# Kernel tuning notes

Measured on AMD Instinct MI355X. Metric: run time of the kernel, lower is better.

The kernel has to match this reference:

```python
import jax, jax.numpy as jnp
import numpy as np

H, C, DK = 4, 63, 64   # n_head, context_size, d_k
NF = H * DK            # n_feat = 256


def setup_inputs() -> dict:
    key = jax.random.key(0)
    ks = jax.random.split(key, 7)
    B, T = 2, 4096
    query = jax.random.normal(ks[0], (B, T, NF), jnp.float32)
    key_t = jax.random.normal(ks[1], (B, T, NF), jnp.float32)   # dummy, unused
    value = jax.random.normal(ks[2], (B, T, NF), jnp.float32)
    mask = jnp.ones((B, 1, T), jnp.bool_)                       # dummy, unused
    s = 1.0 / np.sqrt(NF).astype(np.float32)
    w1 = jax.random.normal(ks[3], (NF, NF), jnp.float32) * s
    w2 = jax.random.normal(ks[4], (H * C, NF), jnp.float32) * s
    w3 = jax.random.normal(ks[5], (NF, NF), jnp.float32) * s
    w_out = jax.random.normal(ks[6], (NF, NF), jnp.float32) * s
    return {"query": query, "key": key_t, "value": value, "mask": mask,
            "w1": w1, "w2": w2, "w3": w3, "w_out": w_out}


def reference(query, key, value, mask, w1, w2, w3, w_out):
    # key and mask are dummies (unused), matching the original module.
    B, T, _ = query.shape
    half = (C - 1) // 2

    q = query @ w1.T                                            # (B,T,NF)
    # synthesized band scores: (B,H,T,C)
    weight = (jax.nn.relu(q) @ w2.T).reshape(B, T, H, C).transpose(0, 2, 1, 3)

    # band geometry: score(i, j) lives at offset k = j - i + half, |j-i| <= half
    j_idx = jnp.arange(T)[:, None] + jnp.arange(C)[None, :] - half   # (T,C)
    valid = (j_idx >= 0) & (j_idx < T)                               # (T,C)
    scores = jnp.where(valid[None, None], weight, -jnp.inf)
    p_attn = jax.nn.softmax(scores, axis=-1)                         # (B,H,T,C)

    v = (value @ w3.T).reshape(B, T, H, DK).transpose(0, 2, 1, 3)    # (B,H,T,DK)
    jc = jnp.clip(j_idx, 0, T - 1)                                   # safe gather idx
    windows = v[:, :, jc, :]                                         # (B,H,T,C,DK)
    x = jnp.einsum('bhtc,bhtcd->bhtd', p_attn, windows)              # (B,H,T,DK)

    x = x.transpose(0, 2, 1, 3).reshape(B, T, NF)
    return x @ w_out.T
```

## Files before the change

kernel.cpp:

```cpp
#include <hip/hip_runtime.h>
#include <hip/hip_bf16.h>
#include <math.h>

typedef _Float16 f16x8 __attribute__((ext_vector_type(8)));
typedef _Float16 f16x4 __attribute__((ext_vector_type(4)));
typedef float    f32x4 __attribute__((ext_vector_type(4)));

__device__ __host__ __forceinline__ int swz(int ch, int row) {
    return (ch & 24) | ((ch & 7) ^ (row & 7));
}
__device__ __forceinline__ f32x4 mfma16(f16x8 a, f16x8 b, f32x4 c) {
    return __builtin_amdgcn_mfma_f32_16x16x32_f16(a, b, c, 0, 0, 0);
}
__device__ __forceinline__ f16x8 cvt8(float4 lo, float4 hi) {
    f16x8 r = { (_Float16)lo.x, (_Float16)lo.y, (_Float16)lo.z, (_Float16)lo.w,
                (_Float16)hi.x, (_Float16)hi.y, (_Float16)hi.z, (_Float16)hi.w };
    return r;
}

__global__ __launch_bounds__(256) void convw(const float* __restrict__ w1,
                                             const float* __restrict__ w2,
                                             const float* __restrict__ w3,
                                             const float* __restrict__ wo,
                                             _Float16* __restrict__ p1,
                                             _Float16* __restrict__ p2,
                                             _Float16* __restrict__ p3,
                                             _Float16* __restrict__ po) {
    int gid = blockIdx.x * 256 + threadIdx.x;
    int widx = gid >> 13;
    int r    = gid & 8191;
    int lane = r & 63;
    int ks   = (r >> 6) & 7;
    int nblk = r >> 9;
    int n  = nblk * 16 + (lane & 15);
    int kc = (ks * 4 + (lane >> 4)) * 8;
    const float* src = widx == 0 ? w1 : widx == 1 ? w2 : widx == 2 ? w3 : wo;
    _Float16*    dst = widx == 0 ? p1 : widx == 1 ? p2 : widx == 2 ? p3 : po;
    f16x8 h = {};
    if (!(widx == 1 && n >= 252)) {
        float4 lo = *(const float4*)&src[n * 256 + kc];
        float4 hi = *(const float4*)&src[n * 256 + kc + 4];
        h = cvt8(lo, hi);
    }
    *(f16x8*)&dst[r * 8] = h;
}

__global__ __launch_bounds__(1024, 4) void mono(const float* __restrict__ query,
                                                const float* __restrict__ value,
                                                const _Float16* __restrict__ w1p,
                                                const _Float16* __restrict__ w2p,
                                                const _Float16* __restrict__ w3p,
                                                const _Float16* __restrict__ wop,
                                                float* __restrict__ outp) {
    __shared__ __align__(16) _Float16 RA[16384];
    __shared__ __align__(16) _Float16 RB[8192];
    __shared__ __align__(16) _Float16 Vs[24576];
    __shared__ __align__(16) _Float16 vwT[26624];

    const int tid = threadIdx.x, lane = tid & 63, wid = tid >> 6;
    const int bidr = blockIdx.x;
    const int work = (bidr & 7) * 32 + (bidr >> 3);
    const int b   = work >> 7;
    const int t0  = (work & 127) * 32;
    const size_t rowb = (size_t)b * 4096;

    _Float16* Aq = RA;
    _Float16* Qr = RA + 8192;
    _Float16* Pl = RA;
    _Float16* sc = RB;
    _Float16* xb = RB;

    {
        int row = tid >> 5, ch = tid & 31;
        const float* qp = &query[(rowb + t0 + row) * 256 + ch * 8];
        float4 qlo = *(const float4*)qp, qhi = *(const float4*)(qp + 4);
        float4 vlo[3], vhi[3];
        #pragma unroll
        for (int it = 0; it < 3; ++it) {
            int slot = it * 1024 + tid;
            int vrow = slot >> 5, vch = slot & 31;
            int jl = t0 - 32 + vrow;
            jl = jl < 0 ? 0 : (jl > 4095 ? 4095 : jl);
            const float* p = &value[(rowb + jl) * 256 + vch * 8];
            vlo[it] = *(const float4*)p;
            vhi[it] = *(const float4*)(p + 4);
        }
        *(f16x8*)&Aq[row * 256 + swz(ch, row) * 8] = cvt8(qlo, qhi);
        #pragma unroll
        for (int it = 0; it < 3; ++it) {
            int slot = it * 1024 + tid;
            int vrow = slot >> 5, vch = slot & 31;
            *(f16x8*)&Vs[vrow * 256 + swz(vch, vrow) * 8] = cvt8(vlo[it], vhi[it]);
        }
    }
    __syncthreads();

    {
        f16x8 bfa[8];
        #pragma unroll
        for (int ks = 0; ks < 8; ++ks)
            bfa[ks] = *(const f16x8*)&w1p[((wid * 8 + ks) * 64 + lane) * 8];
        f32x4 acc[2] = {};
        #pragma unroll
        for (int ks = 0; ks < 8; ++ks) {
            int chn = ks * 4 + (lane >> 4);
            #pragma unroll
            for (int i = 0; i < 2; ++i) {
                int row = i * 16 + (lane & 15);
                f16x8 af = *(const f16x8*)&Aq[row * 256 + swz(chn, row) * 8];
                acc[i] = mfma16(af, bfa[ks], acc[i]);
            }
        }
        const int n = wid * 16 + (lane & 15);
        #pragma unroll
        for (int i = 0; i < 2; ++i)
            #pragma unroll
            for (int r = 0; r < 4; ++r) {
                int row = i * 16 + ((lane >> 4) << 2) + r;
                float v = fmaxf(acc[i][r], 0.f);
                Qr[row * 256 + swz(n >> 3, row) * 8 + (n & 7)] = (_Float16)v;
            }
    }
    __syncthreads();

    {
        f16x8 bfa[8];
        #pragma unroll
        for (int ks = 0; ks < 8; ++ks)
            bfa[ks] = *(const f16x8*)&w2p[((wid * 8 + ks) * 64 + lane) * 8];
        f32x4 acc[2] = {};
        #pragma unroll
        for (int ks = 0; ks < 8; ++ks) {
            int chn = ks * 4 + (lane >> 4);
            #pragma unroll
            for (int i = 0; i < 2; ++i) {
                int row = i * 16 + (lane & 15);
                f16x8 af = *(const f16x8*)&Qr[row * 256 + swz(chn, row) * 8];
                acc[i] = mfma16(af, bfa[ks], acc[i]);
            }
        }
        const int n = wid * 16 + (lane & 15);
        #pragma unroll
        for (int i = 0; i < 2; ++i)
            #pragma unroll
            for (int r = 0; r < 4; ++r) {
                int row = i * 16 + ((lane >> 4) << 2) + r;
                sc[row * 256 + n] = (_Float16)acc[i][r];
            }
    }

    {
        f16x8 bfa[8];
        #pragma unroll
        for (int ks = 0; ks < 8; ++ks)
            bfa[ks] = *(const f16x8*)&w3p[((wid * 8 + ks) * 64 + lane) * 8];
        f32x4 a3[6] = {};
        #pragma unroll
        for (int ks = 0; ks < 8; ++ks) {
            int chn = ks * 4 + (lane >> 4);
            #pragma unroll
            for (int mi = 0; mi < 6; ++mi) {
                int row = mi * 16 + (lane & 15);
                f16x8 af = *(const f16x8*)&Vs[row * 256 + swz(chn, row) * 8];
                a3[mi] = mfma16(af, bfa[ks], a3[mi]);
            }
        }
        const int d = wid * 16 + (lane & 15);
        #pragma unroll
        for (int mi = 0; mi < 6; ++mi) {
            int jw = mi * 16 + ((lane >> 4) << 2);
            f16x4 h = { (_Float16)a3[mi][0], (_Float16)a3[mi][1],
                        (_Float16)a3[mi][2], (_Float16)a3[mi][3] };
            *(f16x4*)&vwT[d * 104 + jw] = h;
        }
    }
    __syncthreads();

    const int h = wid >> 2, q = wid & 3;
    #pragma unroll
    for (int it = 0; it < 2; ++it) {
        int s = it * 64 + lane;
        if (s < 104) {
            int rr = h * 32 + q * 8 + s / 13;
            int cc = s % 13;
            f16x8 z = {};
            *(f16x8*)&Pl[rr * 104 + cc * 8] = z;
        }
    }

    {
        const int hf = lane >> 5, c = lane & 31;
        #pragma unroll
        for (int i = 0; i < 4; ++i) {
            int tl = q * 8 + 2 * i + hf;
            int t  = t0 + tl;
            int c1 = c + 32;
            int j0 = t + c - 31, j1 = t + c1 - 31;
            bool ok0 = (j0 >= 0) && (j0 < 4096);
            bool ok1 = (c1 < 63) && (j1 >= 0) && (j1 < 4096);
            float s0 = ok0 ? (float)sc[tl * 256 + h * 63 + c]  : -INFINITY;
            float s1 = ok1 ? (float)sc[tl * 256 + h * 63 + c1] : -INFINITY;
            float mx = fmaxf(s0, s1);
            #pragma unroll
            for (int off = 16; off > 0; off >>= 1) mx = fmaxf(mx, __shfl_xor(mx, off));
            float e0 = ok0 ? __expf(s0 - mx) : 0.f;
            float e1 = ok1 ? __expf(s1 - mx) : 0.f;
            float sum = e0 + e1;
            #pragma unroll
            for (int off = 16; off > 0; off >>= 1) sum += __shfl_xor(sum, off);
            float inv = 1.0f / sum;
            Pl[(h * 32 + tl) * 104 + (tl + c + 1)] = (_Float16)(e0 * inv);
            if (c1 < 63) Pl[(h * 32 + tl) * 104 + (tl + c1 + 1)] = (_Float16)(e1 * inv);
        }
    }
    __syncthreads();

    {
        const int th = (wid >> 1) & 1, dh = wid & 1;
        f32x4 xa[2] = {};
        #pragma unroll
        for (int ks = 0; ks < 3; ++ks) {
            int chn = ks * 4 + (lane >> 4);
            f16x8 af = *(const f16x8*)&Pl[(h * 32 + th * 16 + (lane & 15)) * 104 + chn * 8];
            #pragma unroll
            for (int j = 0; j < 2; ++j) {
                f16x8 bf = *(const f16x8*)&vwT[(h * 64 + dh * 32 + j * 16 + (lane & 15)) * 104 + chn * 8];
                xa[j] = mfma16(af, bf, xa[j]);
            }
        }
        #pragma unroll
        for (int j = 0; j < 2; ++j)
            #pragma unroll
            for (int r = 0; r < 4; ++r) {
                int row = th * 16 + ((lane >> 4) << 2) + r;
                int n   = h * 64 + dh * 32 + j * 16 + (lane & 15);
                xb[row * 256 + swz(n >> 3, row) * 8 + (n & 7)] = (_Float16)xa[j][r];
            }
    }
    __syncthreads();

    {
        f16x8 bfa[8];
        #pragma unroll
        for (int ks = 0; ks < 8; ++ks)
            bfa[ks] = *(const f16x8*)&wop[((wid * 8 + ks) * 64 + lane) * 8];
        f32x4 oa[2] = {};
        #pragma unroll
        for (int ks = 0; ks < 8; ++ks) {
            int chn = ks * 4 + (lane >> 4);
            #pragma unroll
            for (int i = 0; i < 2; ++i) {
                int row = i * 16 + (lane & 15);
                f16x8 af = *(const f16x8*)&xb[row * 256 + swz(chn, row) * 8];
                oa[i] = mfma16(af, bfa[ks], oa[i]);
            }
        }
        const int n = wid * 16 + (lane & 15);
        #pragma unroll
        for (int i = 0; i < 2; ++i)
            #pragma unroll
            for (int r = 0; r < 4; ++r) {
                int m = t0 + i * 16 + ((lane >> 4) << 2) + r;
                outp[(rowb + m) * 256 + n] = oa[i][r];
            }
    }
}

extern "C" void kernel_launch(void* const* d_in, const int* in_sizes, int n_in,
                              void* d_out, int out_size, void* d_ws, size_t ws_size,
                              hipStream_t stream) {
    const float* query = (const float*)d_in[0];
    const float* value = (const float*)d_in[2];
    const float* w1    = (const float*)d_in[4];
    const float* w2    = (const float*)d_in[5];
    const float* w3    = (const float*)d_in[6];
    const float* w_out = (const float*)d_in[7];

    char* ws = (char*)d_ws;
    _Float16* w1p = (_Float16*)ws;
    _Float16* w2p = w1p + 65536;
    _Float16* w3p = w2p + 65536;
    _Float16* wop = w3p + 65536;

    convw<<<dim3(128), dim3(256), 0, stream>>>(w1, w2, w3, w_out, w1p, w2p, w3p, wop);
    mono<<<dim3(256), dim3(1024), 0, stream>>>(query, value, w1p, w2p, w3p, wop, (float*)d_out);
}
```

Baseline: 25.63 us.

## Fuse weight conversion into main kernel with atomic flag handoff

Removes the separate weight-conversion launch. The first 64 blocks of the main kernel now convert and pack the weights to fp16 and signal completion by incrementing a global atomic counter. Every block spins on that counter after staging its query and value tiles, which hides the conversion behind the input loads. The value projection is also re-tiled so each wave computes 3x2 MFMA tiles instead of 6x1, reusing A fragments across two B fragments. This relies on all producer blocks being co-resident, or the spin-wait can deadlock, and it adds a memset launch.

New measurement: 37.51 us. 1.46x slower.

```diff
diff --git a/kernel.cpp b/kernel.cpp
--- a/kernel.cpp
+++ b/kernel.cpp
@@ -5,6 +5,8 @@
 typedef _Float16 f16x8 __attribute__((ext_vector_type(8)));
 typedef _Float16 f16x4 __attribute__((ext_vector_type(4)));
 typedef float    f32x4 __attribute__((ext_vector_type(4)));
+
+#define NPROD 64
 
 __device__ __host__ __forceinline__ int swz(int ch, int row) {
     return (ch & 24) | ((ch & 7) ^ (row & 7));
@@ -18,39 +20,17 @@
     return r;
 }
 
-__global__ __launch_bounds__(256) void convw(const float* __restrict__ w1,
-                                             const float* __restrict__ w2,
-                                             const float* __restrict__ w3,
-                                             const float* __restrict__ wo,
-                                             _Float16* __restrict__ p1,
-                                             _Float16* __restrict__ p2,
-                                             _Float16* __restrict__ p3,
-                                             _Float16* __restrict__ po) {
-    int gid = blockIdx.x * 256 + threadIdx.x;
-    int widx = gid >> 13;
-    int r    = gid & 8191;
-    int lane = r & 63;
-    int ks   = (r >> 6) & 7;
-    int nblk = r >> 9;
-    int n  = nblk * 16 + (lane & 15);
-    int kc = (ks * 4 + (lane >> 4)) * 8;
-    const float* src = widx == 0 ? w1 : widx == 1 ? w2 : widx == 2 ? w3 : wo;
-    _Float16*    dst = widx == 0 ? p1 : widx == 1 ? p2 : widx == 2 ? p3 : po;
-    f16x8 h = {};
-    if (!(widx == 1 && n >= 252)) {
-        float4 lo = *(const float4*)&src[n * 256 + kc];
-        float4 hi = *(const float4*)&src[n * 256 + kc + 4];
-        h = cvt8(lo, hi);
-    }
-    *(f16x8*)&dst[r * 8] = h;
-}
-
 __global__ __launch_bounds__(1024, 4) void mono(const float* __restrict__ query,
                                                 const float* __restrict__ value,
-                                                const _Float16* __restrict__ w1p,
-                                                const _Float16* __restrict__ w2p,
-                                                const _Float16* __restrict__ w3p,
-                                                const _Float16* __restrict__ wop,
+                                                const float* __restrict__ w1,
+                                                const float* __restrict__ w2,
+                                                const float* __restrict__ w3,
+                                                const float* __restrict__ wo,
+                                                _Float16* __restrict__ w1p,
+                                                _Float16* __restrict__ w2p,
+                                                _Float16* __restrict__ w3p,
+                                                _Float16* __restrict__ wop,
+                                                int* __restrict__ flag,
                                                 float* __restrict__ outp) {
     __shared__ __align__(16) _Float16 RA[16384];
     __shared__ __align__(16) _Float16 RB[8192];
@@ -69,6 +49,30 @@
     _Float16* Pl = RA;
     _Float16* sc = RB;
     _Float16* xb = RB;
+
+    if (bidr < NPROD) {
+        if (tid < 512) {
+            int s = bidr * 512 + tid;
+            int widx = s >> 13, r = s & 8191;
+            int l = r & 63, ks = (r >> 6) & 7, nblk = r >> 9;
+            int n  = nblk * 16 + (l & 15);
+            int kc = (ks * 4 + (l >> 4)) * 8;
+            const float* src = widx == 0 ? w1 : widx == 1 ? w2 : widx == 2 ? w3 : wo;
+            _Float16*    dst = widx == 0 ? w1p : widx == 1 ? w2p : widx == 2 ? w3p : wop;
+            f16x8 h = {};
+            if (!(widx == 1 && n >= 252)) {
+                float4 lo = *(const float4*)&src[n * 256 + kc];
+                float4 hi = *(const float4*)&src[n * 256 + kc + 4];
+                h = cvt8(lo, hi);
+            }
+            *(f16x8*)&dst[r * 8] = h;
+        }
+        __syncthreads();
+        if (tid == 0) {
+            __threadfence();
+            __hip_atomic_fetch_add(flag, 1, __ATOMIC_RELEASE, __HIP_MEMORY_SCOPE_AGENT);
+        }
+    }
 
     {
         int row = tid >> 5, ch = tid & 31;
@@ -95,6 +99,11 @@
     }
     __syncthreads();
 
+    if (tid == 0) {
+        while (__hip_atomic_load(flag, __ATOMIC_ACQUIRE, __HIP_MEMORY_SCOPE_AGENT) < NPROD) { }
+    }
+    __syncthreads();
+
     {
         f16x8 bfa[8];
         #pragma unroll
@@ -150,29 +159,36 @@
     }
 
     {
-        f16x8 bfa[8];
-        #pragma unroll
-        for (int ks = 0; ks < 8; ++ks)
-            bfa[ks] = *(const f16x8*)&w3p[((wid * 8 + ks) * 64 + lane) * 8];
-        f32x4 a3[6] = {};
+        const int rh = wid >> 3, cs = wid & 7;
+        f16x8 bfa0[8], bfa1[8];
+        #pragma unroll
+        for (int ks = 0; ks < 8; ++ks)
+            bfa0[ks] = *(const f16x8*)&w3p[(((cs * 2 + 0) * 8 + ks) * 64 + lane) * 8];
+        #pragma unroll
+        for (int ks = 0; ks < 8; ++ks)
+            bfa1[ks] = *(const f16x8*)&w3p[(((cs * 2 + 1) * 8 + ks) * 64 + lane) * 8];
+        f32x4 a3[3][2] = {};
         #pragma unroll
         for (int ks = 0; ks < 8; ++ks) {
             int chn = ks * 4 + (lane >> 4);
             #pragma unroll
-            for (int mi = 0; mi < 6; ++mi) {
-                int row = mi * 16 + (lane & 15);
+            for (int mi = 0; mi < 3; ++mi) {
+                int row = rh * 48 + mi * 16 + (lane & 15);
                 f16x8 af = *(const f16x8*)&Vs[row * 256 + swz(chn, row) * 8];
-                a3[mi] = mfma16(af, bfa[ks], a3[mi]);
-            }
-        }
-        const int d = wid * 16 + (lane & 15);
-        #pragma unroll
-        for (int mi = 0; mi < 6; ++mi) {
-            int jw = mi * 16 + ((lane >> 4) << 2);
-            f16x4 h = { (_Float16)a3[mi][0], (_Float16)a3[mi][1],
-                        (_Float16)a3[mi][2], (_Float16)a3[mi][3] };
-            *(f16x4*)&vwT[d * 104 + jw] = h;
-        }
+                a3[mi][0] = mfma16(af, bfa0[ks], a3[mi][0]);
+                a3[mi][1] = mfma16(af, bfa1[ks], a3[mi][1]);
+            }
+        }
+        #pragma unroll
+        for (int mi = 0; mi < 3; ++mi)
+            #pragma unroll
+            for (int j = 0; j < 2; ++j) {
+                int d  = cs * 32 + j * 16 + (lane & 15);
+                int jw = rh * 48 + mi * 16 + ((lane >> 4) << 2);
+                f16x4 h = { (_Float16)a3[mi][j][0], (_Float16)a3[mi][j][1],
+                            (_Float16)a3[mi][j][2], (_Float16)a3[mi][j][3] };
+                *(f16x4*)&vwT[d * 104 + jw] = h;
+            }
     }
     __syncthreads();
 
@@ -281,7 +297,9 @@
     _Float16* w2p = w1p + 65536;
     _Float16* w3p = w2p + 65536;
     _Float16* wop = w3p + 65536;
-
-    convw<<<dim3(128), dim3(256), 0, stream>>>(w1, w2, w3, w_out, w1p, w2p, w3p, wop);
-    mono<<<dim3(256), dim3(1024), 0, stream>>>(query, value, w1p, w2p, w3p, wop, (float*)d_out);
-}
+    int* flag = (int*)(ws + 512 * 1024);
+
+    hipMemsetAsync(flag, 0, 4, stream);
+    mono<<<dim3(256), dim3(1024), 0, stream>>>(query, value, w1, w2, w3, w_out,
+                                               w1p, w2p, w3p, wop, flag, (float*)d_out);
+}
```

## Overlap value loads with early GEMMs and retile the value projection

Applied to the files above, without the earlier changes.

Moves the w1 weight fragment loads ahead of the first barrier. The barriers now wait only on LDS/scalar counters (lgkmcnt), so the global value loads can stay in flight while the query projection and score GEMMs run. The fp16 conversion and LDS store of the value tile are deferred until just before the value projection. That projection is retiled so each wave computes a 3x2 block of MFMA tiles, reusing each A fragment for two B fragments. The costs are higher register pressure from holding the value data and two sets of w3 fragments, and the removal of the barrier after the vwT writes.

Result: slower. 27.10 us (+5.7%).

```diff
diff --git a/kernel.cpp b/kernel.cpp
--- a/kernel.cpp
+++ b/kernel.cpp
@@ -16,6 +16,11 @@
     f16x8 r = { (_Float16)lo.x, (_Float16)lo.y, (_Float16)lo.z, (_Float16)lo.w,
                 (_Float16)hi.x, (_Float16)hi.y, (_Float16)hi.z, (_Float16)hi.w };
     return r;
+}
+__device__ __forceinline__ void barrier_lgkm() {
+    asm volatile("s_waitcnt lgkmcnt(0)" ::: "memory");
+    __builtin_amdgcn_s_barrier();
+    __builtin_amdgcn_sched_barrier(0);
 }
 
 __global__ __launch_bounds__(256) void convw(const float* __restrict__ w1,
@@ -70,11 +75,12 @@
     _Float16* sc = RB;
     _Float16* xb = RB;
 
+    float4 vlo[3], vhi[3];
+    f16x8 bfa1g[8];
     {
         int row = tid >> 5, ch = tid & 31;
         const float* qp = &query[(rowb + t0 + row) * 256 + ch * 8];
         float4 qlo = *(const float4*)qp, qhi = *(const float4*)(qp + 4);
-        float4 vlo[3], vhi[3];
         #pragma unroll
         for (int it = 0; it < 3; ++it) {
             int slot = it * 1024 + tid;
@@ -85,21 +91,14 @@
             vlo[it] = *(const float4*)p;
             vhi[it] = *(const float4*)(p + 4);
         }
+        #pragma unroll
+        for (int ks = 0; ks < 8; ++ks)
+            bfa1g[ks] = *(const f16x8*)&w1p[((wid * 8 + ks) * 64 + lane) * 8];
         *(f16x8*)&Aq[row * 256 + swz(ch, row) * 8] = cvt8(qlo, qhi);
-        #pragma unroll
-        for (int it = 0; it < 3; ++it) {
-            int slot = it * 1024 + tid;
-            int vrow = slot >> 5, vch = slot & 31;
-            *(f16x8*)&Vs[vrow * 256 + swz(vch, vrow) * 8] = cvt8(vlo[it], vhi[it]);
-        }
-    }
-    __syncthreads();
-
-    {
-        f16x8 bfa[8];
-        #pragma unroll
-        for (int ks = 0; ks < 8; ++ks)
-            bfa[ks] = *(const f16x8*)&w1p[((wid * 8 + ks) * 64 + lane) * 8];
+    }
+    barrier_lgkm();
+
+    {
         f32x4 acc[2] = {};
         #pragma unroll
         for (int ks = 0; ks < 8; ++ks) {
@@ -108,7 +107,7 @@
             for (int i = 0; i < 2; ++i) {
                 int row = i * 16 + (lane & 15);
                 f16x8 af = *(const f16x8*)&Aq[row * 256 + swz(chn, row) * 8];
-                acc[i] = mfma16(af, bfa[ks], acc[i]);
+                acc[i] = mfma16(af, bfa1g[ks], acc[i]);
             }
         }
         const int n = wid * 16 + (lane & 15);
@@ -121,7 +120,7 @@
                 Qr[row * 256 + swz(n >> 3, row) * 8 + (n & 7)] = (_Float16)v;
             }
     }
-    __syncthreads();
+    barrier_lgkm();
 
     {
         f16x8 bfa[8];
@@ -149,32 +148,46 @@
             }
     }
 
-    {
-        f16x8 bfa[8];
-        #pragma unroll
-        for (int ks = 0; ks < 8; ++ks)
-            bfa[ks] = *(const f16x8*)&w3p[((wid * 8 + ks) * 64 + lane) * 8];
-        f32x4 a3[6] = {};
-        #pragma unroll
-        for (int ks = 0; ks < 8; ++ks) {
-            int chn = ks * 4 + (lane >> 4);
-            #pragma unroll
-            for (int mi = 0; mi < 6; ++mi) {
-                int row = mi * 16 + (lane & 15);
+    #pragma unroll
+    for (int it = 0; it < 3; ++it) {
+        int slot = it * 1024 + tid;
+        int vrow = slot >> 5, vch = slot & 31;
+        *(f16x8*)&Vs[vrow * 256 + swz(vch, vrow) * 8] = cvt8(vlo[it], vhi[it]);
+    }
+    __syncthreads();
+
+    {
+        const int rh = wid >> 3, cs = wid & 7;
+        f16x8 bfa0[8], bfa1[8];
+        #pragma unroll
+        for (int ks = 0; ks < 8; ++ks)
+            bfa0[ks] = *(const f16x8*)&w3p[(((cs * 2 + 0) * 8 + ks) * 64 + lane) * 8];
+        #pragma unroll
+        for (int ks = 0; ks < 8; ++ks)
+            bfa1[ks] = *(const f16x8*)&w3p[(((cs * 2 + 1) * 8 + ks) * 64 + lane) * 8];
+        f32x4 a3[3][2] = {};
+        #pragma unroll
+        for (int ks = 0; ks < 8; ++ks) {
+            int chn = ks * 4 + (lane >> 4);
+            #pragma unroll
+            for (int mi = 0; mi < 3; ++mi) {
+                int row = rh * 48 + mi * 16 + (lane & 15);
                 f16x8 af = *(const f16x8*)&Vs[row * 256 + swz(chn, row) * 8];
-                a3[mi] = mfma16(af, bfa[ks], a3[mi]);
-            }
-        }
-        const int d = wid * 16 + (lane & 15);
-        #pragma unroll
-        for (int mi = 0; mi < 6; ++mi) {
-            int jw = mi * 16 + ((lane >> 4) << 2);
-            f16x4 h = { (_Float16)a3[mi][0], (_Float16)a3[mi][1],
-                        (_Float16)a3[mi][2], (_Float16)a3[mi][3] };
-            *(f16x4*)&vwT[d * 104 + jw] = h;
-        }
-    }
-    __syncthreads();
+                a3[mi][0] = mfma16(af, bfa0[ks], a3[mi][0]);
+                a3[mi][1] = mfma16(af, bfa1[ks], a3[mi][1]);
+            }
+        }
+        #pragma unroll
+        for (int mi = 0; mi < 3; ++mi)
+            #pragma unroll
+            for (int j = 0; j < 2; ++j) {
+                int d  = cs * 32 + j * 16 + (lane & 15);
+                int jw = rh * 48 + mi * 16 + ((lane >> 4) << 2);
+                f16x4 h = { (_Float16)a3[mi][j][0], (_Float16)a3[mi][j][1],
+                            (_Float16)a3[mi][j][2], (_Float16)a3[mi][j][3] };
+                *(f16x4*)&vwT[d * 104 + jw] = h;
+            }
+    }
 
     const int h = wid >> 2, q = wid & 3;
     #pragma unroll
@@ -187,7 +200,6 @@
             *(f16x8*)&Pl[rr * 104 + cc * 8] = z;
         }
     }
-
     {
         const int hf = lane >> 5, c = lane & 31;
         #pragma unroll
```
